# Kernel tuning notes

Measured on AMD Instinct MI355X. Metric: run time of the kernel, lower is better.

Reference implementation:

```python
import jax, jax.numpy as jnp
import numpy as np

B = 8192      # graphs per batch
NPG = 40      # nodes per graph (= average_nodes, uniform here)
DEG = 16      # avg degree
IN = 64
HID = 32
OUT = 10
K1 = 20       # ceil(0.5*40)
K2 = 10       # ceil(0.5*20)
N = B * NPG
E = N * DEG
EPS = 1e-15


def _lin_params(k, fi, fo):
    kw, kb = jax.random.split(k)
    s = 1.0 / np.sqrt(fi)
    w = jax.random.uniform(kw, (fi, fo), jnp.float32, -s, s)
    b = jax.random.uniform(kb, (fo,), jnp.float32, -s, s)
    return w, b


def setup_inputs():
    key = jax.random.key(0)
    ks = jax.random.split(key, 14)
    x = jax.random.normal(ks[0], (N, IN), jnp.float32)
    # edges constrained within each graph (graphs are contiguous blocks of NPG nodes)
    g = jnp.repeat(jnp.arange(B, dtype=jnp.int32), NPG * DEG)
    src = g * NPG + jax.random.randint(ks[1], (E,), 0, NPG, dtype=jnp.int32)
    dst = g * NPG + jax.random.randint(ks[2], (E,), 0, NPG, dtype=jnp.int32)
    edge_index = jnp.stack([src, dst])
    batch = jnp.repeat(jnp.arange(B, dtype=jnp.int32), NPG)
    w_c1, b_c1 = _lin_params(ks[3], IN, HID)
    w_p1, b_p1 = _lin_params(ks[4], HID, K1)
    w2r, b2 = _lin_params(ks[5], HID, HID)
    w2o, _ = _lin_params(ks[6], HID, HID)
    w_p2, b_p2 = _lin_params(ks[7], HID, K2)
    w3r, b3 = _lin_params(ks[8], HID, HID)
    w3o, _ = _lin_params(ks[9], HID, HID)
    w_l1, b_l1 = _lin_params(ks[10], HID, HID)
    w_l2, b_l2 = _lin_params(ks[11], HID, OUT)
    return dict(x=x, edge_index=edge_index, batch=batch,
                w_c1=w_c1, b_c1=b_c1, w_p1=w_p1, b_p1=b_p1,
                w2r=w2r, b2=b2, w2o=w2o, w_p2=w_p2, b_p2=b_p2,
                w3r=w3r, b3=b3, w3o=w3o,
                w_l1=w_l1, b_l1=b_l1, w_l2=w_l2, b_l2=b_l2)


def _gcn_conv(x, edge_index, w, b):
    # PyG GCNConv: x' = D^-1/2 (A + I) D^-1/2 (X W) + b, unit edge weights
    h = x @ w
    row, col = edge_index
    deg = jnp.zeros((N,), h.dtype).at[col].add(1.0) + 1.0  # +1 self loop
    dinv = jax.lax.rsqrt(deg)
    msg = (dinv[row] * dinv[col])[:, None] * h[row]
    out = jnp.zeros_like(h).at[col].add(msg)
    out = out + (dinv * dinv)[:, None] * h  # self-loop contribution
    return out + b


def _dense_mincut_pool(x, adj, s, mask=None):
    # faithful to torch_geometric.nn.dense_mincut_pool
    s = jax.nn.softmax(s, axis=-1)
    if mask is not None:
        m = mask[..., None].astype(x.dtype)
        x = x * m
        s = s * m
    k = s.shape[-1]
    out = jnp.einsum('bnk,bnf->bkf', s, x)
    out_adj = jnp.einsum('bnk,bnm,bml->bkl', s, adj, s)
    mincut_num = jnp.trace(out_adj, axis1=1, axis2=2)
    d_flat = adj.sum(-1)                                   # [B, n]
    mincut_den = jnp.einsum('bnk,bn,bnk->b', s, d_flat, s)  # tr(S^T D S)
    mincut_loss = jnp.mean(-(mincut_num / mincut_den))
    ss = jnp.einsum('bnk,bnl->bkl', s, s)
    ss_norm = jnp.sqrt(jnp.sum(ss * ss, axis=(1, 2), keepdims=True))
    i_s = jnp.eye(k, dtype=x.dtype) / jnp.sqrt(jnp.asarray(k, x.dtype))
    ortho_loss = jnp.mean(jnp.sqrt(jnp.sum((ss / ss_norm - i_s) ** 2, axis=(1, 2))))
    # zero diagonal, then symmetric degree-normalize coarse adjacency
    eye = jnp.eye(k, dtype=x.dtype)
    out_adj = out_adj * (1.0 - eye)
    d = jnp.sqrt(out_adj.sum(-1))[:, None, :] + EPS        # [B,1,k]
    out_adj = out_adj / d / jnp.swapaxes(d, 1, 2)
    return out, out_adj, mincut_loss, ortho_loss


def _dense_graph_conv(x, adj, w_rel, b, w_root):
    # PyG DenseGraphConv (aggr='add'): lin_rel(A @ x) + lin_root(x); lin_root bias=False
    return (adj @ x) @ w_rel + b + x @ w_root


def reference(x, edge_index, batch, w_c1, b_c1, w_p1, b_p1, w2r, b2, w2o,
              w_p2, b_p2, w3r, b3, w3o, w_l1, b_l1, w_l2, b_l2):
    h = jax.nn.relu(_gcn_conv(x, edge_index, w_c1, b_c1))
    # to_dense_batch (uniform NPG nodes per graph, batch sorted)
    local = jnp.arange(N, dtype=jnp.int32) - batch * NPG
    xd = jnp.zeros((B, NPG, HID), h.dtype).at[batch, local].set(h)
    mask = jnp.ones((B, NPG), bool)
    # to_dense_adj (accumulates duplicate edges)
    row, col = edge_index
    g = batch[row]
    adj = jnp.zeros((B, NPG, NPG), h.dtype).at[g, row - g * NPG, col - g * NPG].add(1.0)
    s = xd @ w_p1 + b_p1
    xd, adj, mc1, o1 = _dense_mincut_pool(xd, adj, s, mask)
    xd = jax.nn.relu(_dense_graph_conv(xd, adj, w2r, b2, w2o))
    s = xd @ w_p2 + b_p2
    xd, adj, mc2, o2 = _dense_mincut_pool(xd, adj, s)
    xd = _dense_graph_conv(xd, adj, w3r, b3, w3o)
    pooled = xd.mean(axis=1)
    out = jax.nn.relu(pooled @ w_l1 + b_l1) @ w_l2 + b_l2
    return out, mc1 + mc2 + o1 + o2
```

## Files before the change

kernel.cpp:

```cpp
#include <hip/hip_runtime.h>

#define NT 256

constexpr int Bg   = 8192;
constexpr int NPG  = 40;
constexpr int EPG  = 640;
constexpr int IN_  = 64;
constexpr int HID  = 32;
constexpr int K1   = 20;
constexpr int K2   = 10;
constexpr int OUTC = 10;
constexpr int NE   = Bg * NPG * 16;
constexpr int SH   = 36;
constexpr float EPSF = 1e-15f;

#define FMA4(acc, a, b) do { \
    float _s = (a); \
    acc.x = fmaf(_s, (b).x, acc.x); \
    acc.y = fmaf(_s, (b).y, acc.y); \
    acc.z = fmaf(_s, (b).z, acc.z); \
    acc.w = fmaf(_s, (b).w, acc.w); } while (0)

__device__ __forceinline__ float wave_red(float v) {
#pragma unroll
    for (int off = 32; off > 0; off >>= 1) v += __shfl_down(v, off, 64);
    return v;
}

__global__ __launch_bounds__(NT, 4)
void mincut_fused(const float* __restrict__ x, const int* __restrict__ ei,
                  const float* __restrict__ w_c1, const float* __restrict__ b_c1,
                  const float* __restrict__ w_p1, const float* __restrict__ b_p1,
                  const float* __restrict__ w2r_, const float* __restrict__ b2_,
                  const float* __restrict__ w2o_,
                  const float* __restrict__ w_p2, const float* __restrict__ b_p2,
                  const float* __restrict__ w3r_, const float* __restrict__ b3_,
                  const float* __restrict__ w3o_,
                  const float* __restrict__ w_l1, const float* __restrict__ b_l1,
                  const float* __restrict__ w_l2, const float* __restrict__ b_l2,
                  float* __restrict__ out, float* __restrict__ wsg)
{
    __shared__ __align__(16) float sA_[NPG * NPG];
    __shared__ __align__(16) float bufH[NPG * SH];
    __shared__ __align__(16) float bufXd[NPG * SH];
    __shared__ __align__(16) float bufS[NPG * K1];
    __shared__ __align__(16) float bufAS[NPG * K1];
    __shared__ __align__(16) float sSS[K1 * K1];
    __shared__ __align__(16) float sdinv[NPG];
    __shared__ __align__(16) float srowsA[NPG];
    __shared__ __align__(16) float srowm[NPG];
    __shared__ __align__(16) float sden[NPG];
    __shared__ __align__(16) float sred1[2];
    __shared__ __align__(16) float sred2[2];
    __shared__ __align__(16) float sc[8];

    float* sA2  = sA_;
    float* sX2  = bufH;
    float* sW2r = bufH + 720;
    float* sW2o = bufAS;
    float* sS2  = bufS;
    float* sAS2 = bufS + 200;
    float* sA3  = bufS + 400;
    float* sSS2 = bufS + 500;
    float* sW3r = bufXd;
    float* sW3o = bufXd + 360;
    float* sX3  = bufXd + 720;
    float* sX4  = bufXd + 1080;

    const int g    = blockIdx.x;
    const int tid  = threadIdx.x;
    const int lane = tid & 63;
    const int wid  = tid >> 6;

    int er0, ec0, er1, ec1, er2 = -1, ec2 = 0;
    {
        const int eb = g * EPG, nb = g * NPG;
        const int* srcp = ei;
        const int* dstp = ei + NE;
        int e = eb + tid;
        er0 = srcp[e] - nb; ec0 = dstp[e] - nb;
        e += NT;
        er1 = srcp[e] - nb; ec1 = dstp[e] - nb;
        if (tid + 2 * NT < EPG) {
            e += NT;
            er2 = srcp[e] - nb; ec2 = dstp[e] - nb;
        }
    }
    for (int i = tid; i < NPG * NPG; i += NT) sA_[i] = 0.f;
    __syncthreads();

    atomicAdd(&sA_[er0 * NPG + ec0], 1.f);
    atomicAdd(&sA_[er1 * NPG + ec1], 1.f);
    if (er2 >= 0) atomicAdd(&sA_[er2 * NPG + ec2], 1.f);

    if (tid < 160) {
        int np = tid >> 3, fq = tid & 7;
        int n0 = 2 * np, n1 = n0 + 1;
        const float4* x0 = (const float4*)(x + (size_t)g * (NPG * IN_) + n0 * IN_);
        const float4* x1 = (const float4*)(x + (size_t)g * (NPG * IN_) + n1 * IN_);
        const float4* wg = (const float4*)w_c1;
        float4 acc0 = {0.f,0.f,0.f,0.f}, acc1 = {0.f,0.f,0.f,0.f};
#pragma unroll 4
        for (int kk = 0; kk < IN_ / 4; kk++) {
            float4 a0 = x0[kk], a1 = x1[kk];
            float4 w0 = wg[(4*kk+0)*8 + fq];
            float4 w1 = wg[(4*kk+1)*8 + fq];
            float4 w2 = wg[(4*kk+2)*8 + fq];
            float4 w3 = wg[(4*kk+3)*8 + fq];
            FMA4(acc0, a0.x, w0); FMA4(acc0, a0.y, w1);
            FMA4(acc0, a0.z, w2); FMA4(acc0, a0.w, w3);
            FMA4(acc1, a1.x, w0); FMA4(acc1, a1.y, w1);
            FMA4(acc1, a1.z, w2); FMA4(acc1, a1.w, w3);
        }
        ((float4*)(bufH + n0 * SH))[fq] = acc0;
        ((float4*)(bufH + n1 * SH))[fq] = acc1;
    }
    __syncthreads();

    if (tid < NPG) {
        float s = 0.f;
#pragma unroll
        for (int r = 0; r < NPG; r++) s += sA_[r * NPG + tid];
        sdinv[tid] = rsqrtf(s + 1.f);
    } else if (tid >= 64 && tid < 64 + NPG) {
        int n = tid - 64; float s = 0.f;
#pragma unroll
        for (int m = 0; m < NPG; m++) s += sA_[n * NPG + m];
        srowsA[n] = s;
    }
    __syncthreads();

    if (tid < 160) {
        int cp = tid >> 3, fq = tid & 7;
        int c0 = 2 * cp, c1 = c0 + 1;
        float4 acc0 = {0.f,0.f,0.f,0.f}, acc1 = {0.f,0.f,0.f,0.f};
#pragma unroll 8
        for (int r = 0; r < NPG; r++) {
            float2 a2 = *(const float2*)&sA_[r * NPG + c0];
            float dv = sdinv[r];
            float4 b = ((const float4*)(bufH + r * SH))[fq];
            FMA4(acc0, a2.x * dv, b);
            FMA4(acc1, a2.y * dv, b);
        }
        float4 bb = ((const float4*)b_c1)[fq];
        float4 h0 = ((const float4*)(bufH + c0 * SH))[fq];
        float4 h1 = ((const float4*)(bufH + c1 * SH))[fq];
        float d0 = sdinv[c0], d1 = sdinv[c1];
        float4 r0, r1;
        r0.x = fmaxf(fmaf(d0, fmaf(d0, h0.x, acc0.x), bb.x), 0.f);
        r0.y = fmaxf(fmaf(d0, fmaf(d0, h0.y, acc0.y), bb.y), 0.f);
        r0.z = fmaxf(fmaf(d0, fmaf(d0, h0.z, acc0.z), bb.z), 0.f);
        r0.w = fmaxf(fmaf(d0, fmaf(d0, h0.w, acc0.w), bb.w), 0.f);
        r1.x = fmaxf(fmaf(d1, fmaf(d1, h1.x, acc1.x), bb.x), 0.f);
        r1.y = fmaxf(fmaf(d1, fmaf(d1, h1.y, acc1.y), bb.y), 0.f);
        r1.z = fmaxf(fmaf(d1, fmaf(d1, h1.z, acc1.z), bb.z), 0.f);
        r1.w = fmaxf(fmaf(d1, fmaf(d1, h1.w, acc1.w), bb.w), 0.f);
        ((float4*)(bufXd + c0 * SH))[fq] = r0;
        ((float4*)(bufXd + c1 * SH))[fq] = r1;
    }
    __syncthreads();

    if (tid < 100) {
        int np = tid / 5, lq = tid - np * 5;
        int n0 = 2 * np, n1 = n0 + 1;
        const float4* wg = (const float4*)w_p1;
        float4 bb = ((const float4*)b_p1)[lq];
        float4 acc0 = bb, acc1 = bb;
#pragma unroll 8
        for (int k = 0; k < HID; k++) {
            float a0 = bufXd[n0 * SH + k];
            float a1 = bufXd[n1 * SH + k];
            float4 w = wg[k * 5 + lq];
            FMA4(acc0, a0, w);
            FMA4(acc1, a1, w);
        }
        ((float4*)(bufS + n0 * K1))[lq] = acc0;
        ((float4*)(bufS + n1 * K1))[lq] = acc1;
    }
    __syncthreads();

    if (tid < NPG) {
        float* row = bufS + tid * K1;
        float v[K1]; float m = -3.0e38f;
#pragma unroll
        for (int k = 0; k < K1; k++) { v[k] = row[k]; m = fmaxf(m, v[k]); }
        float ssum = 0.f;
#pragma unroll
        for (int k = 0; k < K1; k++) { v[k] = __expf(v[k] - m); ssum += v[k]; }
        float inv = 1.f / ssum;
#pragma unroll
        for (int k = 0; k < K1; k++) row[k] = v[k] * inv;
    }
    __syncthreads();

    if (tid < 100) {
        int np = tid / 5, lq = tid - np * 5;
        int n0 = 2 * np, n1 = n0 + 1;
        const float4* sb = (const float4*)bufS;
        float4 acc0 = {0.f,0.f,0.f,0.f}, acc1 = {0.f,0.f,0.f,0.f};
#pragma unroll
        for (int m4 = 0; m4 < NPG / 4; m4++) {
            float4 a0 = *(const float4*)&sA_[n0 * NPG + 4 * m4];
            float4 a1 = *(const float4*)&sA_[n1 * NPG + 4 * m4];
            float4 b0 = sb[(4*m4+0)*5 + lq];
            float4 b1 = sb[(4*m4+1)*5 + lq];
            float4 b2v = sb[(4*m4+2)*5 + lq];
            float4 b3v = sb[(4*m4+3)*5 + lq];
            FMA4(acc0, a0.x, b0); FMA4(acc0, a0.y, b1);
            FMA4(acc0, a0.z, b2v); FMA4(acc0, a0.w, b3v);
            FMA4(acc1, a1.x, b0); FMA4(acc1, a1.y, b1);
            FMA4(acc1, a1.z, b2v); FMA4(acc1, a1.w, b3v);
        }
        ((float4*)(bufAS + n0 * K1))[lq] = acc0;
        ((float4*)(bufAS + n1 * K1))[lq] = acc1;
    } else if (tid < 150) {
        int oo = tid - 100;
        int kp = oo / 5, lq = oo - kp * 5;
        int k0 = 2 * kp, k1 = k0 + 1;
        float4 acc0 = {0.f,0.f,0.f,0.f}, acc1 = {0.f,0.f,0.f,0.f};
#pragma unroll 8
        for (int n = 0; n < NPG; n++) {
            float2 s2v = *(const float2*)&bufS[n * K1 + k0];
            float4 b = ((const float4*)(bufS + n * K1))[lq];
            FMA4(acc0, s2v.x, b);
            FMA4(acc1, s2v.y, b);
        }
        ((float4*)(sSS + k0 * K1))[lq] = acc0;
        ((float4*)(sSS + k1 * K1))[lq] = acc1;
    }
    __syncthreads();

    if (tid < 50) {
        int kp = tid / 5, lq = tid - kp * 5;
        int k0 = 2 * kp, k1 = k0 + 1;
        float4 acc0 = {0.f,0.f,0.f,0.f}, acc1 = {0.f,0.f,0.f,0.f};
#pragma unroll 8
        for (int n = 0; n < NPG; n++) {
            float2 s2v = *(const float2*)&bufS[n * K1 + k0];
            float4 b = ((const float4*)(bufAS + n * K1))[lq];
            FMA4(acc0, s2v.x, b);
            FMA4(acc1, s2v.y, b);
        }
        ((float4*)(sA2 + k0 * K1))[lq] = acc0;
        ((float4*)(sA2 + k1 * K1))[lq] = acc1;
    } else if (tid < 130) {
        int oo = tid - 50;
        int kp = oo >> 3, fq = oo & 7;
        int k0 = 2 * kp, k1 = k0 + 1;
        float4 acc0 = {0.f,0.f,0.f,0.f}, acc1 = {0.f,0.f,0.f,0.f};
#pragma unroll 8
        for (int n = 0; n < NPG; n++) {
            float2 s2v = *(const float2*)&bufS[n * K1 + k0];
            float4 b = ((const float4*)(bufXd + n * SH))[fq];
            FMA4(acc0, s2v.x, b);
            FMA4(acc1, s2v.y, b);
        }
        ((float4*)(sX2 + k0 * SH))[fq] = acc0;
        ((float4*)(sX2 + k1 * SH))[fq] = acc1;
    } else if (tid < 170) {
        int n = tid - 130;
        float s2 = 0.f;
#pragma unroll
        for (int k = 0; k < K1; k++) { float v = bufS[n * K1 + k]; s2 = fmaf(v, v, s2); }
        sden[n] = srowsA[n] * s2;
    } else if (wid == 3) {
        float v = 0.f;
        for (int i = lane; i < K1 * K1; i += 64) { float t = sSS[i]; v = fmaf(t, t, v); }
        v = wave_red(v); if (lane == 0) sc[2] = v;
    }
    __syncthreads();

    if (wid < 2) {
        float rn = 1.f / sqrtf(sc[2]);
        const float isk = 0.22360679774997896f;
        float p = 0.f;
        for (int o = tid; o < K1 * K1; o += 128) {
            int k = o / K1, l = o - k * K1;
            float v = sSS[o] * rn - ((k == l) ? isk : 0.f);
            p = fmaf(v, v, p);
        }
        p = wave_red(p);
        if (lane == 0) sred1[wid] = p;
    } else if (wid == 2) {
        float v = (lane < K1) ? sA2[lane * (K1 + 1)] : 0.f;
        v = wave_red(v); if (lane == 0) sc[0] = v;
        if (lane < K1) {
            float s = 0.f;
#pragma unroll
            for (int l = 0; l < K1; l++) s += sA2[lane * K1 + l];
            s -= sA2[lane * (K1 + 1)];
            srowm[lane] = 1.f / (sqrtf(s) + EPSF);
        }
    } else {
        float v = (lane < NPG) ? sden[lane] : 0.f;
        v = wave_red(v); if (lane == 0) sc[1] = v;
    }
    for (int o = tid; o < 320; o += NT) {
        bool first = (o < 160);
        int oo = first ? o : o - 160;
        int n = oo >> 3, fq = oo & 7;
        const float4* wg = (const float4*)(first ? w2r_ : w2o_);
        float4 acc = {0.f,0.f,0.f,0.f};
#pragma unroll 8
        for (int k = 0; k < HID; k++) {
            float a = sX2[n * SH + k];
            FMA4(acc, a, wg[k * 8 + fq]);
        }
        if (first) ((float4*)(sW2r + n * SH))[fq] = acc;
        else       ((float4*)(sW2o + n * SH))[fq] = acc;
    }
    __syncthreads();

    if (tid < 80) {
        int kp = tid >> 3, fq = tid & 7;
        int k0 = 2 * kp, k1 = k0 + 1;
        float4 acc0 = {0.f,0.f,0.f,0.f}, acc1 = {0.f,0.f,0.f,0.f};
#pragma unroll
        for (int l = 0; l < K1; l++) {
            float rl = srowm[l];
            float a0 = (l == k0) ? 0.f : sA2[k0 * K1 + l];
            float a1 = (l == k1) ? 0.f : sA2[k1 * K1 + l];
            float4 w = ((const float4*)(sW2r + l * SH))[fq];
            FMA4(acc0, a0 * rl, w);
            FMA4(acc1, a1 * rl, w);
        }
        float4 bb = ((const float4*)b2_)[fq];
        float4 o0 = ((const float4*)(sW2o + k0 * SH))[fq];
        float4 o1 = ((const float4*)(sW2o + k1 * SH))[fq];
        float rk0 = srowm[k0], rk1 = srowm[k1];
        float4 r0, r1;
        r0.x = fmaxf(fmaf(rk0, acc0.x, o0.x + bb.x), 0.f);
        r0.y = fmaxf(fmaf(rk0, acc0.y, o0.y + bb.y), 0.f);
        r0.z = fmaxf(fmaf(rk0, acc0.z, o0.z + bb.z), 0.f);
        r0.w = fmaxf(fmaf(rk0, acc0.w, o0.w + bb.w), 0.f);
        r1.x = fmaxf(fmaf(rk1, acc1.x, o1.x + bb.x), 0.f);
        r1.y = fmaxf(fmaf(rk1, acc1.y, o1.y + bb.y), 0.f);
        r1.z = fmaxf(fmaf(rk1, acc1.z, o1.z + bb.z), 0.f);
        r1.w = fmaxf(fmaf(rk1, acc1.w, o1.w + bb.w), 0.f);
        ((float4*)(sX2 + k0 * SH))[fq] = r0;
        ((float4*)(sX2 + k1 * SH))[fq] = r1;
    }
    __syncthreads();

    if (tid < K1 * K2) {
        int n = tid / K2, q = tid - n * K2;
        float acc = b_p2[q];
#pragma unroll 8
        for (int j = 0; j < HID; j++) acc = fmaf(sX2[n * SH + j], w_p2[j * K2 + q], acc);
        sS2[tid] = acc;
    }
    __syncthreads();

    if (tid < K1) {
        float* row = sS2 + tid * K2;
        float v[K2]; float m = -3.0e38f;
#pragma unroll
        for (int q = 0; q < K2; q++) { v[q] = row[q]; m = fmaxf(m, v[q]); }
        float ssum = 0.f;
#pragma unroll
        for (int q = 0; q < K2; q++) { v[q] = __expf(v[q] - m); ssum += v[q]; }
        float inv = 1.f / ssum;
#pragma unroll
        for (int q = 0; q < K2; q++) row[q] = v[q] * inv;
    }
    __syncthreads();

    for (int o = tid; o < 400; o += NT) {
        if (o < 200) {
            int n = o / K2, l = o - n * K2;
            float acc = 0.f;
#pragma unroll
            for (int m = 0; m < K1; m++) {
                float a = (m == n) ? 0.f : sA2[n * K1 + m];
                acc = fmaf(a * srowm[m], sS2[m * K2 + l], acc);
            }
            sAS2[n * K2 + l] = acc * srowm[n];
        } else if (o < 300) {
            int oo = o - 200; int k = oo / K2, l = oo - k * K2;
            float acc = 0.f;
#pragma unroll
            for (int n = 0; n < K1; n++) acc = fmaf(sS2[n * K2 + k], sS2[n * K2 + l], acc);
            sSS2[k * K2 + l] = acc;
        } else if (o < 380) {
            int oo = o - 300; int k = oo >> 3, fq = oo & 7;
            float4 acc = {0.f, 0.f, 0.f, 0.f};
#pragma unroll
            for (int n = 0; n < K1; n++) {
                float a = sS2[n * K2 + k];
                float4 b = ((const float4*)(sX2 + n * SH))[fq];
                FMA4(acc, a, b);
            }
            ((float4*)(sX3 + k * SH))[fq] = acc;
        } else {
            int n = o - 380;
            float da = 0.f, s2 = 0.f;
#pragma unroll
            for (int l = 0; l < K1; l++) {
                float a = (l == n) ? 0.f : sA2[n * K1 + l];
                da = fmaf(a, srowm[l], da);
            }
            da *= srowm[n];
#pragma unroll
            for (int q = 0; q < K2; q++) { float v = sS2[n * K2 + q]; s2 = fmaf(v, v, s2); }
            sden[n] = da * s2;
        }
    }
    __syncthreads();

    if (tid < K2 * K2) {
        int k = tid / K2, l = tid - k * K2;
        float acc = 0.f;
#pragma unroll
        for (int n = 0; n < K1; n++) acc = fmaf(sS2[n * K2 + k], sAS2[n * K2 + l], acc);
        sA3[tid] = acc;
    } else if (wid == 2) {
        float v = (lane < K1) ? sden[lane] : 0.f;
        v = wave_red(v); if (lane == 0) sc[5] = v;
    } else if (wid == 3) {
        float v = 0.f;
        for (int i = lane; i < K2 * K2; i += 64) { float t = sSS2[i]; v = fmaf(t, t, v); }
        v = wave_red(v); if (lane == 0) sc[6] = v;
    }
    __syncthreads();

    if (wid == 0) {
        float rn = 1.f / sqrtf(sc[6]);
        const float isk = 0.31622776601683794f;
        float p = 0.f;
        for (int i = lane; i < K2 * K2; i += 64) {
            int k = i / K2, l = i - k * K2;
            float v = sSS2[i] * rn - ((k == l) ? isk : 0.f);
            p = fmaf(v, v, p);
        }
        p = wave_red(p);
        if (lane == 0) sred2[0] = p;
    } else if (wid == 1) {
        float v = (lane < K2) ? sA3[lane * (K2 + 1)] : 0.f;
        v = wave_red(v); if (lane == 0) sc[4] = v;
        if (lane < K2) {
            float s = 0.f;
#pragma unroll
            for (int l = 0; l < K2; l++) s += sA3[lane * K2 + l];
            s -= sA3[lane * (K2 + 1)];
            srowm[lane] = 1.f / (sqrtf(s) + EPSF);
        }
    }
    __syncthreads();

    if (tid < 160) {
        bool first = (tid < 80);
        int oo = first ? tid : tid - 80;
        int n = oo >> 3, fq = oo & 7;
        const float4* wg = (const float4*)(first ? w3r_ : w3o_);
        float4 acc = {0.f,0.f,0.f,0.f};
#pragma unroll 8
        for (int k = 0; k < HID; k++) {
            float a = sX3[n * SH + k];
            FMA4(acc, a, wg[k * 8 + fq]);
        }
        if (first) ((float4*)(sW3r + n * SH))[fq] = acc;
        else       ((float4*)(sW3o + n * SH))[fq] = acc;
    } else if (tid == 200) {
        float o1 = sqrtf(sred1[0] + sred1[1]);
        float o2 = sqrtf(sred2[0]);
        wsg[g] = -(sc[0] / sc[1]) + o1 - (sc[4] / sc[5]) + o2;
    }
    __syncthreads();

    if (tid < 40) {
        int kp = tid >> 3, fq = tid & 7;
        int k0 = 2 * kp, k1 = k0 + 1;
        float4 acc0 = {0.f,0.f,0.f,0.f}, acc1 = {0.f,0.f,0.f,0.f};
#pragma unroll
        for (int l = 0; l < K2; l++) {
            float rl = srowm[l];
            float a0 = (l == k0) ? 0.f : sA3[k0 * K2 + l];
            float a1 = (l == k1) ? 0.f : sA3[k1 * K2 + l];
            float4 w = ((const float4*)(sW3r + l * SH))[fq];
            FMA4(acc0, a0 * rl, w);
            FMA4(acc1, a1 * rl, w);
        }
        float4 bb = ((const float4*)b3_)[fq];
        float4 o0 = ((const float4*)(sW3o + k0 * SH))[fq];
        float4 o1 = ((const float4*)(sW3o + k1 * SH))[fq];
        float rk0 = srowm[k0], rk1 = srowm[k1];
        float4 r0, r1;
        r0.x = fmaf(rk0, acc0.x, o0.x + bb.x);
        r0.y = fmaf(rk0, acc0.y, o0.y + bb.y);
        r0.z = fmaf(rk0, acc0.z, o0.z + bb.z);
        r0.w = fmaf(rk0, acc0.w, o0.w + bb.w);
        r1.x = fmaf(rk1, acc1.x, o1.x + bb.x);
        r1.y = fmaf(rk1, acc1.y, o1.y + bb.y);
        r1.z = fmaf(rk1, acc1.z, o1.z + bb.z);
        r1.w = fmaf(rk1, acc1.w, o1.w + bb.w);
        ((float4*)(sX4 + k0 * SH))[fq] = r0;
        ((float4*)(sX4 + k1 * SH))[fq] = r1;
    }
    __syncthreads();

    if (wid == 0) {
        int f = lane & 31;
        float pool = 0.f;
#pragma unroll
        for (int n = 0; n < K2; n++) pool += sX4[n * SH + f];
        pool *= (1.f / K2);
        float acc = b_l1[f];
#pragma unroll
        for (int j = 0; j < HID; j++)
            acc = fmaf(__shfl(pool, j, 64), w_l1[j * HID + f], acc);
        float t1 = fmaxf(acc, 0.f);
        int o = (lane < OUTC) ? lane : 0;
        float acc2 = b_l2[o];
#pragma unroll
        for (int j = 0; j < HID; j++)
            acc2 = fmaf(__shfl(t1, j, 64), w_l2[j * OUTC + o], acc2);
        if (lane < OUTC) out[(size_t)g * OUTC + lane] = acc2;
    }
}

__global__ void loss_reduce(const float* __restrict__ wsg, float* __restrict__ out)
{
    __shared__ float sred[4];
    int tid = threadIdx.x;
    float s = 0.f;
    for (int i = tid; i < Bg; i += NT) s += wsg[i];
    s = wave_red(s);
    if ((tid & 63) == 0) sred[tid >> 6] = s;
    __syncthreads();
    if (tid == 0) out[(size_t)Bg * OUTC] = (sred[0] + sred[1] + sred[2] + sred[3]) * (1.f / Bg);
}

extern "C" void kernel_launch(void* const* d_in, const int* in_sizes, int n_in,
                              void* d_out, int out_size, void* d_ws, size_t ws_size,
                              hipStream_t stream)
{
    const float* x    = (const float*)d_in[0];
    const int*   ei   = (const int*)  d_in[1];
    const float* w_c1 = (const float*)d_in[3];
    const float* b_c1 = (const float*)d_in[4];
    const float* w_p1 = (const float*)d_in[5];
    const float* b_p1 = (const float*)d_in[6];
    const float* w2r  = (const float*)d_in[7];
    const float* b2   = (const float*)d_in[8];
    const float* w2o  = (const float*)d_in[9];
    const float* w_p2 = (const float*)d_in[10];
    const float* b_p2 = (const float*)d_in[11];
    const float* w3r  = (const float*)d_in[12];
    const float* b3   = (const float*)d_in[13];
    const float* w3o  = (const float*)d_in[14];
    const float* w_l1 = (const float*)d_in[15];
    const float* b_l1 = (const float*)d_in[16];
    const float* w_l2 = (const float*)d_in[17];
    const float* b_l2 = (const float*)d_in[18];
    float* out = (float*)d_out;
    float* wsg = (float*)d_ws;

    hipLaunchKernelGGL(mincut_fused, dim3(Bg), dim3(NT), 0, stream,
                       x, ei, w_c1, b_c1, w_p1, b_p1, w2r, b2, w2o,
                       w_p2, b_p2, w3r, b3, w3o, w_l1, b_l1, w_l2, b_l2,
                       out, wsg);
    hipLaunchKernelGGL(loss_reduce, dim3(1), dim3(NT), 0, stream, wsg, out);
}
```

Before: 286.1 us.

## Process two graphs per block with a unified shared-memory arena

Each 256-thread block now handles two graphs instead of one, looping work items over both graphs so that idle threads in small phases are put to use. Shared memory becomes one flat arena with fixed offsets per graph, and the x tile is staged into LDS with coalesced float4 loads before the first linear layer. Several reductions are restructured into half-wave reductions and per-thread partial sums. The arena roughly doubles LDS per block (about 53 KB), which may cut occupancy, and the kernel launches half as many blocks.

New measurement: 314.9 us. +10.1%, slower.

```diff
diff --git a/kernel.cpp b/kernel.cpp
--- a/kernel.cpp
+++ b/kernel.cpp
@@ -14,12 +14,43 @@
 constexpr int SH   = 36;
 constexpr float EPSF = 1e-15f;
 
+constexpr int R = 6672;
+constexpr int AOFF   = 0;
+constexpr int HOFF   = 1600;
+constexpr int X2OFF  = 1600;
+constexpr int W2ROFF = 2320;
+constexpr int XdOFF  = 3040;
+constexpr int XOFF   = 3040;
+constexpr int W3ROFF = 3040;
+constexpr int W3OOFF = 3400;
+constexpr int X3OFF  = 3760;
+constexpr int X4OFF  = 4120;
+constexpr int SOFF   = 4480;
+constexpr int S2OFF  = 4480;
+constexpr int AS2OFF = 4680;
+constexpr int A3OFF  = 4880;
+constexpr int SS2OFF = 4980;
+constexpr int ASOFF  = 5280;
+constexpr int W2OOFF = 5280;
+constexpr int SSOFF  = 6080;
+constexpr int DINV   = 6480;
+constexpr int ROWSA  = 6520;
+constexpr int ROWM   = 6560;
+constexpr int SDEN   = 6600;
+constexpr int SC     = 6640;
+
 #define FMA4(acc, a, b) do { \
     float _s = (a); \
     acc.x = fmaf(_s, (b).x, acc.x); \
     acc.y = fmaf(_s, (b).y, acc.y); \
     acc.z = fmaf(_s, (b).z, acc.z); \
     acc.w = fmaf(_s, (b).w, acc.w); } while (0)
+
+__device__ __forceinline__ float hred32(float v) {
+#pragma unroll
+    for (int off = 16; off > 0; off >>= 1) v += __shfl_down(v, off, 32);
+    return v;
+}
 
 __device__ __forceinline__ float wave_red(float v) {
 #pragma unroll
@@ -40,64 +71,43 @@
                   const float* __restrict__ w_l2, const float* __restrict__ b_l2,
                   float* __restrict__ out, float* __restrict__ wsg)
 {
-    __shared__ __align__(16) float sA_[NPG * NPG];
-    __shared__ __align__(16) float bufH[NPG * SH];
-    __shared__ __align__(16) float bufXd[NPG * SH];
-    __shared__ __align__(16) float bufS[NPG * K1];
-    __shared__ __align__(16) float bufAS[NPG * K1];
-    __shared__ __align__(16) float sSS[K1 * K1];
-    __shared__ __align__(16) float sdinv[NPG];
-    __shared__ __align__(16) float srowsA[NPG];
-    __shared__ __align__(16) float srowm[NPG];
-    __shared__ __align__(16) float sden[NPG];
-    __shared__ __align__(16) float sred1[2];
-    __shared__ __align__(16) float sred2[2];
-    __shared__ __align__(16) float sc[8];
-
-    float* sA2  = sA_;
-    float* sX2  = bufH;
-    float* sW2r = bufH + 720;
-    float* sW2o = bufAS;
-    float* sS2  = bufS;
-    float* sAS2 = bufS + 200;
-    float* sA3  = bufS + 400;
-    float* sSS2 = bufS + 500;
-    float* sW3r = bufXd;
-    float* sW3o = bufXd + 360;
-    float* sX3  = bufXd + 720;
-    float* sX4  = bufXd + 1080;
-
-    const int g    = blockIdx.x;
+    __shared__ __align__(16) float sm[2 * R];
+
+    const int b    = blockIdx.x;
     const int tid  = threadIdx.x;
     const int lane = tid & 63;
     const int wid  = tid >> 6;
-
-    int er0, ec0, er1, ec1, er2 = -1, ec2 = 0;
+    const int hl   = tid & 31;
+    const int hw   = tid >> 5;
+
+    int aoff[5];
     {
-        const int eb = g * EPG, nb = g * NPG;
-        const int* srcp = ei;
-        const int* dstp = ei + NE;
-        int e = eb + tid;
-        er0 = srcp[e] - nb; ec0 = dstp[e] - nb;
-        e += NT;
-        er1 = srcp[e] - nb; ec1 = dstp[e] - nb;
-        if (tid + 2 * NT < EPG) {
-            e += NT;
-            er2 = srcp[e] - nb; ec2 = dstp[e] - nb;
-        }
-    }
-    for (int i = tid; i < NPG * NPG; i += NT) sA_[i] = 0.f;
-    __syncthreads();
-
-    atomicAdd(&sA_[er0 * NPG + ec0], 1.f);
-    atomicAdd(&sA_[er1 * NPG + ec1], 1.f);
-    if (er2 >= 0) atomicAdd(&sA_[er2 * NPG + ec2], 1.f);
-
-    if (tid < 160) {
-        int np = tid >> 3, fq = tid & 7;
-        int n0 = 2 * np, n1 = n0 + 1;
-        const float4* x0 = (const float4*)(x + (size_t)g * (NPG * IN_) + n0 * IN_);
-        const float4* x1 = (const float4*)(x + (size_t)g * (NPG * IN_) + n1 * IN_);
+        const int gi = tid >> 7;
+        const int nb = (2 * b + gi) * NPG;
+        const int base = gi * R;
+        const int e0 = b * 1280 + tid * 5;
+#pragma unroll
+        for (int j = 0; j < 5; j++) {
+            int r = ei[e0 + j] - nb, c = ei[NE + e0 + j] - nb;
+            aoff[j] = base + r * NPG + c;
+        }
+    }
+    for (int o = tid; o < 3200; o += NT) sm[(o < 1600) ? o : (R + o - 1600)] = 0.f;
+    for (int o = tid; o < 1280; o += NT) {
+        int gi = o >= 640; int i = o - 640 * gi;
+        int n = i >> 4, k = i & 15;
+        ((float4*)(sm + gi * R + XOFF + n * 68))[k] =
+            ((const float4*)(x + (size_t)(2 * b + gi) * (NPG * IN_)))[i];
+    }
+    __syncthreads();
+
+#pragma unroll
+    for (int j = 0; j < 5; j++) atomicAdd(&sm[aoff[j]], 1.f);
+    for (int o = tid; o < 320; o += NT) {
+        int gi = o >= 160; int oo = o - 160 * gi; float* G = sm + gi * R;
+        int np = oo >> 3, fq = oo & 7, n0 = 2 * np, n1 = n0 + 1;
+        const float4* x0 = (const float4*)(G + XOFF + n0 * 68);
+        const float4* x1 = (const float4*)(G + XOFF + n1 * 68);
         const float4* wg = (const float4*)w_c1;
         float4 acc0 = {0.f,0.f,0.f,0.f}, acc1 = {0.f,0.f,0.f,0.f};
 #pragma unroll 4
@@ -112,40 +122,43 @@
             FMA4(acc1, a1.x, w0); FMA4(acc1, a1.y, w1);
             FMA4(acc1, a1.z, w2); FMA4(acc1, a1.w, w3);
         }
-        ((float4*)(bufH + n0 * SH))[fq] = acc0;
-        ((float4*)(bufH + n1 * SH))[fq] = acc1;
-    }
-    __syncthreads();
-
-    if (tid < NPG) {
-        float s = 0.f;
-#pragma unroll
-        for (int r = 0; r < NPG; r++) s += sA_[r * NPG + tid];
-        sdinv[tid] = rsqrtf(s + 1.f);
-    } else if (tid >= 64 && tid < 64 + NPG) {
-        int n = tid - 64; float s = 0.f;
-#pragma unroll
-        for (int m = 0; m < NPG; m++) s += sA_[n * NPG + m];
-        srowsA[n] = s;
-    }
-    __syncthreads();
-
-    if (tid < 160) {
-        int cp = tid >> 3, fq = tid & 7;
-        int c0 = 2 * cp, c1 = c0 + 1;
+        ((float4*)(G + HOFF + n0 * SH))[fq] = acc0;
+        ((float4*)(G + HOFF + n1 * SH))[fq] = acc1;
+    }
+    __syncthreads();
+
+    for (int o = tid; o < 160; o += NT) {
+        int gi = o >= 80; int oo = o - 80 * gi; float* G = sm + gi * R;
+        if (oo < NPG) {
+            float s = 0.f;
+#pragma unroll
+            for (int r = 0; r < NPG; r++) s += G[r * NPG + oo];
+            G[DINV + oo] = rsqrtf(s + 1.f);
+        } else {
+            int n = oo - NPG; float s = 0.f;
+#pragma unroll
+            for (int m = 0; m < NPG; m++) s += G[n * NPG + m];
+            G[ROWSA + n] = s;
+        }
+    }
+    __syncthreads();
+
+    for (int o = tid; o < 320; o += NT) {
+        int gi = o >= 160; int oo = o - 160 * gi; float* G = sm + gi * R;
+        int cp = oo >> 3, fq = oo & 7, c0 = 2 * cp, c1 = c0 + 1;
         float4 acc0 = {0.f,0.f,0.f,0.f}, acc1 = {0.f,0.f,0.f,0.f};
 #pragma unroll 8
         for (int r = 0; r < NPG; r++) {
-            float2 a2 = *(const float2*)&sA_[r * NPG + c0];
-            float dv = sdinv[r];
-            float4 b = ((const float4*)(bufH + r * SH))[fq];
-            FMA4(acc0, a2.x * dv, b);
-            FMA4(acc1, a2.y * dv, b);
+            float2 a2 = *(const float2*)&G[r * NPG + c0];
+            float dv = G[DINV + r];
+            float4 bv = ((const float4*)(G + HOFF + r * SH))[fq];
+            FMA4(acc0, a2.x * dv, bv);
+            FMA4(acc1, a2.y * dv, bv);
         }
         float4 bb = ((const float4*)b_c1)[fq];
-        float4 h0 = ((const float4*)(bufH + c0 * SH))[fq];
-        float4 h1 = ((const float4*)(bufH + c1 * SH))[fq];
-        float d0 = sdinv[c0], d1 = sdinv[c1];
+        float4 h0 = ((const float4*)(G + HOFF + c0 * SH))[fq];
+        float4 h1 = ((const float4*)(G + HOFF + c1 * SH))[fq];
+        float d0 = G[DINV + c0], d1 = G[DINV + c1];
         float4 r0, r1;
         r0.x = fmaxf(fmaf(d0, fmaf(d0, h0.x, acc0.x), bb.x), 0.f);
         r0.y = fmaxf(fmaf(d0, fmaf(d0, h0.y, acc0.y), bb.y), 0.f);
@@ -155,32 +168,32 @@
         r1.y = fmaxf(fmaf(d1, fmaf(d1, h1.y, acc1.y), bb.y), 0.f);
         r1.z = fmaxf(fmaf(d1, fmaf(d1, h1.z, acc1.z), bb.z), 0.f);
         r1.w = fmaxf(fmaf(d1, fmaf(d1, h1.w, acc1.w), bb.w), 0.f);
-        ((float4*)(bufXd + c0 * SH))[fq] = r0;
-        ((float4*)(bufXd + c1 * SH))[fq] = r1;
-    }
-    __syncthreads();
-
-    if (tid < 100) {
-        int np = tid / 5, lq = tid - np * 5;
-        int n0 = 2 * np, n1 = n0 + 1;
+        ((float4*)(G + XdOFF + c0 * SH))[fq] = r0;
+        ((float4*)(G + XdOFF + c1 * SH))[fq] = r1;
+    }
+    __syncthreads();
+
+    for (int o = tid; o < 200; o += NT) {
+        int gi = o >= 100; int oo = o - 100 * gi; float* G = sm + gi * R;
+        int np = oo / 5, lq = oo - np * 5, n0 = 2 * np, n1 = n0 + 1;
         const float4* wg = (const float4*)w_p1;
         float4 bb = ((const float4*)b_p1)[lq];
         float4 acc0 = bb, acc1 = bb;
 #pragma unroll 8
         for (int k = 0; k < HID; k++) {
-            float a0 = bufXd[n0 * SH + k];
-            float a1 = bufXd[n1 * SH + k];
+            float a0 = G[XdOFF + n0 * SH + k];
+            float a1 = G[XdOFF + n1 * SH + k];
             float4 w = wg[k * 5 + lq];
-            FMA4(acc0, a0, w);
-            FMA4(acc1, a1, w);
-        }
-        ((float4*)(bufS + n0 * K1))[lq] = acc0;
-        ((float4*)(bufS + n1 * K1))[lq] = acc1;
-    }
-    __syncthreads();
-
-    if (tid < NPG) {
-        float* row = bufS + tid * K1;
+            FMA4(acc0, a0, w); FMA4(acc1, a1, w);
+        }
+        ((float4*)(G + SOFF + n0 * K1))[lq] = acc0;
+        ((float4*)(G + SOFF + n1 * K1))[lq] = acc1;
+    }
+    __syncthreads();
+
+    if (tid < 80) {
+        int gi = tid >= 40; int n = tid - 40 * gi;
+        float* row = sm + gi * R + SOFF + n * K1;
         float v[K1]; float m = -3.0e38f;
 #pragma unroll
         for (int k = 0; k < K1; k++) { v[k] = row[k]; m = fmaxf(m, v[k]); }
@@ -193,141 +206,139 @@
     }
     __syncthreads();
 
-    if (tid < 100) {
-        int np = tid / 5, lq = tid - np * 5;
-        int n0 = 2 * np, n1 = n0 + 1;
-        const float4* sb = (const float4*)bufS;
-        float4 acc0 = {0.f,0.f,0.f,0.f}, acc1 = {0.f,0.f,0.f,0.f};
-#pragma unroll
-        for (int m4 = 0; m4 < NPG / 4; m4++) {
-            float4 a0 = *(const float4*)&sA_[n0 * NPG + 4 * m4];
-            float4 a1 = *(const float4*)&sA_[n1 * NPG + 4 * m4];
-            float4 b0 = sb[(4*m4+0)*5 + lq];
-            float4 b1 = sb[(4*m4+1)*5 + lq];
-            float4 b2v = sb[(4*m4+2)*5 + lq];
-            float4 b3v = sb[(4*m4+3)*5 + lq];
-            FMA4(acc0, a0.x, b0); FMA4(acc0, a0.y, b1);
-            FMA4(acc0, a0.z, b2v); FMA4(acc0, a0.w, b3v);
-            FMA4(acc1, a1.x, b0); FMA4(acc1, a1.y, b1);
-            FMA4(acc1, a1.z, b2v); FMA4(acc1, a1.w, b3v);
-        }
-        ((float4*)(bufAS + n0 * K1))[lq] = acc0;
-        ((float4*)(bufAS + n1 * K1))[lq] = acc1;
-    } else if (tid < 150) {
-        int oo = tid - 100;
-        int kp = oo / 5, lq = oo - kp * 5;
-        int k0 = 2 * kp, k1 = k0 + 1;
-        float4 acc0 = {0.f,0.f,0.f,0.f}, acc1 = {0.f,0.f,0.f,0.f};
-#pragma unroll 8
-        for (int n = 0; n < NPG; n++) {
-            float2 s2v = *(const float2*)&bufS[n * K1 + k0];
-            float4 b = ((const float4*)(bufS + n * K1))[lq];
-            FMA4(acc0, s2v.x, b);
-            FMA4(acc1, s2v.y, b);
-        }
-        ((float4*)(sSS + k0 * K1))[lq] = acc0;
-        ((float4*)(sSS + k1 * K1))[lq] = acc1;
-    }
-    __syncthreads();
-
-    if (tid < 50) {
-        int kp = tid / 5, lq = tid - kp * 5;
-        int k0 = 2 * kp, k1 = k0 + 1;
-        float4 acc0 = {0.f,0.f,0.f,0.f}, acc1 = {0.f,0.f,0.f,0.f};
-#pragma unroll 8
-        for (int n = 0; n < NPG; n++) {
-            float2 s2v = *(const float2*)&bufS[n * K1 + k0];
-            float4 b = ((const float4*)(bufAS + n * K1))[lq];
-            FMA4(acc0, s2v.x, b);
-            FMA4(acc1, s2v.y, b);
-        }
-        ((float4*)(sA2 + k0 * K1))[lq] = acc0;
-        ((float4*)(sA2 + k1 * K1))[lq] = acc1;
-    } else if (tid < 130) {
-        int oo = tid - 50;
-        int kp = oo >> 3, fq = oo & 7;
-        int k0 = 2 * kp, k1 = k0 + 1;
-        float4 acc0 = {0.f,0.f,0.f,0.f}, acc1 = {0.f,0.f,0.f,0.f};
-#pragma unroll 8
-        for (int n = 0; n < NPG; n++) {
-            float2 s2v = *(const float2*)&bufS[n * K1 + k0];
-            float4 b = ((const float4*)(bufXd + n * SH))[fq];
-            FMA4(acc0, s2v.x, b);
-            FMA4(acc1, s2v.y, b);
-        }
-        ((float4*)(sX2 + k0 * SH))[fq] = acc0;
-        ((float4*)(sX2 + k1 * SH))[fq] = acc1;
-    } else if (tid < 170) {
-        int n = tid - 130;
-        float s2 = 0.f;
-#pragma unroll
-        for (int k = 0; k < K1; k++) { float v = bufS[n * K1 + k]; s2 = fmaf(v, v, s2); }
-        sden[n] = srowsA[n] * s2;
-    } else if (wid == 3) {
+    for (int o = tid; o < 300; o += NT) {
+        int gi = o >= 150; int oo = o - 150 * gi; float* G = sm + gi * R;
+        if (oo < 100) {
+            int np = oo / 5, lq = oo - np * 5, n0 = 2 * np, n1 = n0 + 1;
+            const float4* sb = (const float4*)(G + SOFF);
+            float4 acc0 = {0.f,0.f,0.f,0.f}, acc1 = {0.f,0.f,0.f,0.f};
+#pragma unroll
+            for (int m4 = 0; m4 < NPG / 4; m4++) {
+                float4 a0 = *(const float4*)&G[n0 * NPG + 4 * m4];
+                float4 a1 = *(const float4*)&G[n1 * NPG + 4 * m4];
+                float4 b0 = sb[(4*m4+0)*5 + lq];
+                float4 b1 = sb[(4*m4+1)*5 + lq];
+                float4 b2v = sb[(4*m4+2)*5 + lq];
+                float4 b3v = sb[(4*m4+3)*5 + lq];
+                FMA4(acc0, a0.x, b0); FMA4(acc0, a0.y, b1);
+                FMA4(acc0, a0.z, b2v); FMA4(acc0, a0.w, b3v);
+                FMA4(acc1, a1.x, b0); FMA4(acc1, a1.y, b1);
+                FMA4(acc1, a1.z, b2v); FMA4(acc1, a1.w, b3v);
+            }
+            ((float4*)(G + ASOFF + n0 * K1))[lq] = acc0;
+            ((float4*)(G + ASOFF + n1 * K1))[lq] = acc1;
+        } else {
+            int m = oo - 100;
+            int kp = m / 5, lq = m - kp * 5, k0 = 2 * kp, k1 = k0 + 1;
+            float4 acc0 = {0.f,0.f,0.f,0.f}, acc1 = {0.f,0.f,0.f,0.f};
+#pragma unroll 8
+            for (int n = 0; n < NPG; n++) {
+                float2 s2v = *(const float2*)&G[SOFF + n * K1 + k0];
+                float4 bv = ((const float4*)(G + SOFF + n * K1))[lq];
+                FMA4(acc0, s2v.x, bv); FMA4(acc1, s2v.y, bv);
+            }
+            ((float4*)(G + SSOFF + k0 * K1))[lq] = acc0;
+            ((float4*)(G + SSOFF + k1 * K1))[lq] = acc1;
+        }
+    }
+    __syncthreads();
+
+    for (int o = tid; o < 340; o += NT) {
+        int gi = o >= 170; int oo = o - 170 * gi; float* G = sm + gi * R;
+        if (oo < 50) {
+            int kp = oo / 5, lq = oo - kp * 5, k0 = 2 * kp, k1 = k0 + 1;
+            float4 acc0 = {0.f,0.f,0.f,0.f}, acc1 = {0.f,0.f,0.f,0.f};
+#pragma unroll 8
+            for (int n = 0; n < NPG; n++) {
+                float2 s2v = *(const float2*)&G[SOFF + n * K1 + k0];
+                float4 bv = ((const float4*)(G + ASOFF + n * K1))[lq];
+                FMA4(acc0, s2v.x, bv); FMA4(acc1, s2v.y, bv);
+            }
+            ((float4*)(G + AOFF + k0 * K1))[lq] = acc0;
+            ((float4*)(G + AOFF + k1 * K1))[lq] = acc1;
+        } else if (oo < 130) {
+            int m = oo - 50;
+            int kp = m >> 3, fq = m & 7, k0 = 2 * kp, k1 = k0 + 1;
+            float4 acc0 = {0.f,0.f,0.f,0.f}, acc1 = {0.f,0.f,0.f,0.f};
+#pragma unroll 8
+            for (int n = 0; n < NPG; n++) {
+                float2 s2v = *(const float2*)&G[SOFF + n * K1 + k0];
+                float4 bv = ((const float4*)(G + XdOFF + n * SH))[fq];
+                FMA4(acc0, s2v.x, bv); FMA4(acc1, s2v.y, bv);
+            }
+            ((float4*)(G + X2OFF + k0 * SH))[fq] = acc0;
+            ((float4*)(G + X2OFF + k1 * SH))[fq] = acc1;
+        } else {
+            int n = oo - 130;
+            float s2 = 0.f;
+#pragma unroll
+            for (int k = 0; k < K1; k++) { float v = G[SOFF + n * K1 + k]; s2 = fmaf(v, v, s2); }
+            G[SDEN + n] = G[ROWSA + n] * s2;
+        }
+    }
+    __syncthreads();
+
+    if (hw < 2) {
+        float* G = sm + hw * R;
+        float f = 0.f, tr = 0.f;
+        for (int i = hl; i < K1 * K1; i += 32) {
+            float t = G[SSOFF + i];
+            f = fmaf(t, t, f);
+            if (i % (K1 + 1) == 0) tr += t;
+        }
+        f = hred32(f); tr = hred32(tr);
+        if (hl == 0)
+            G[SC + 2] = sqrtf(fmaxf(2.f - 2.f * tr / (sqrtf(f) * 4.47213595499958f), 0.f));
+    } else if (hw < 4) {
+        float* G = sm + (hw - 2) * R;
         float v = 0.f;
-        for (int i = lane; i < K1 * K1; i += 64) { float t = sSS[i]; v = fmaf(t, t, v); }
-        v = wave_red(v); if (lane == 0) sc[2] = v;
-    }
-    __syncthreads();
-
-    if (wid < 2) {
-        float rn = 1.f / sqrtf(sc[2]);
-        const float isk = 0.22360679774997896f;
-        float p = 0.f;
-        for (int o = tid; o < K1 * K1; o += 128) {
-            int k = o / K1, l = o - k * K1;
-            float v = sSS[o] * rn - ((k == l) ? isk : 0.f);
-            p = fmaf(v, v, p);
-        }
-        p = wave_red(p);
-        if (lane == 0) sred1[wid] = p;
-    } else if (wid == 2) {
-        float v = (lane < K1) ? sA2[lane * (K1 + 1)] : 0.f;
-        v = wave_red(v); if (lane == 0) sc[0] = v;
-        if (lane < K1) {
+        if (hl < K1) {
             float s = 0.f;
 #pragma unroll
-            for (int l = 0; l < K1; l++) s += sA2[lane * K1 + l];
-            s -= sA2[lane * (K1 + 1)];
-            srowm[lane] = 1.f / (sqrtf(s) + EPSF);
-        }
-    } else {
-        float v = (lane < NPG) ? sden[lane] : 0.f;
-        v = wave_red(v); if (lane == 0) sc[1] = v;
-    }
-    for (int o = tid; o < 320; o += NT) {
-        bool first = (o < 160);
-        int oo = first ? o : o - 160;
-        int n = oo >> 3, fq = oo & 7;
+            for (int l = 0; l < K1; l++) s += G[AOFF + hl * K1 + l];
+            float d = G[AOFF + hl * (K1 + 1)];
+            G[ROWM + hl] = 1.f / (sqrtf(s - d) + EPSF);
+            v = d;
+        }
+        v = hred32(v);
+        if (hl == 0) G[SC + 0] = v;
+    } else if (hw < 6) {
+        float* G = sm + (hw - 4) * R;
+        float v = G[SDEN + hl] + ((hl < 8) ? G[SDEN + hl + 32] : 0.f);
+        v = hred32(v);
+        if (hl == 0) G[SC + 1] = v;
+    }
+    for (int o = tid; o < 640; o += NT) {
+        int gi = o >= 320; int oo = o - 320 * gi; float* G = sm + gi * R;
+        int first = oo < 160; int m = first ? oo : oo - 160;
+        int n = m >> 3, fq = m & 7;
         const float4* wg = (const float4*)(first ? w2r_ : w2o_);
         float4 acc = {0.f,0.f,0.f,0.f};
 #pragma unroll 8
         for (int k = 0; k < HID; k++) {
-            float a = sX2[n * SH + k];
+            float a = G[X2OFF + n * SH + k];
             FMA4(acc, a, wg[k * 8 + fq]);
         }
-        if (first) ((float4*)(sW2r + n * SH))[fq] = acc;
-        else       ((float4*)(sW2o + n * SH))[fq] = acc;
-    }
-    __syncthreads();
-
-    if (tid < 80) {
-        int kp = tid >> 3, fq = tid & 7;
-        int k0 = 2 * kp, k1 = k0 + 1;
+        ((float4*)(G + (first ? W2ROFF : W2OOFF) + n * SH))[fq] = acc;
+    }
+    __syncthreads();
+
+    for (int o = tid; o < 160; o += NT) {
+        int gi = o >= 80; int oo = o - 80 * gi; float* G = sm + gi * R;
+        int kp = oo >> 3, fq = oo & 7, k0 = 2 * kp, k1 = k0 + 1;
         float4 acc0 = {0.f,0.f,0.f,0.f}, acc1 = {0.f,0.f,0.f,0.f};
 #pragma unroll
         for (int l = 0; l < K1; l++) {
-            float rl = srowm[l];
-            float a0 = (l == k0) ? 0.f : sA2[k0 * K1 + l];
-            float a1 = (l == k1) ? 0.f : sA2[k1 * K1 + l];
-            float4 w = ((const float4*)(sW2r + l * SH))[fq];
-            FMA4(acc0, a0 * rl, w);
-            FMA4(acc1, a1 * rl, w);
+            float rl = G[ROWM + l];
+            float a0 = (l == k0) ? 0.f : G[AOFF + k0 * K1 + l];
+            float a1 = (l == k1) ? 0.f : G[AOFF + k1 * K1 + l];
+            float4 w = ((const float4*)(G + W2ROFF + l * SH))[fq];
+            FMA4(acc0, a0 * rl, w); FMA4(acc1, a1 * rl, w);
         }
         float4 bb = ((const float4*)b2_)[fq];
-        float4 o0 = ((const float4*)(sW2o + k0 * SH))[fq];
-        float4 o1 = ((const float4*)(sW2o + k1 * SH))[fq];
-        float rk0 = srowm[k0], rk1 = srowm[k1];
+        float4 o0 = ((const float4*)(G + W2OOFF + k0 * SH))[fq];
+        float4 o1 = ((const float4*)(G + W2OOFF + k1 * SH))[fq];
+        float rk0 = G[ROWM + k0], rk1 = G[ROWM + k1];
         float4 r0, r1;
         r0.x = fmaxf(fmaf(rk0, acc0.x, o0.x + bb.x), 0.f);
         r0.y = fmaxf(fmaf(rk0, acc0.y, o0.y + bb.y), 0.f);
@@ -337,22 +348,24 @@
         r1.y = fmaxf(fmaf(rk1, acc1.y, o1.y + bb.y), 0.f);
         r1.z = fmaxf(fmaf(rk1, acc1.z, o1.z + bb.z), 0.f);
         r1.w = fmaxf(fmaf(rk1, acc1.w, o1.w + bb.w), 0.f);
-        ((float4*)(sX2 + k0 * SH))[fq] = r0;
-        ((float4*)(sX2 + k1 * SH))[fq] = r1;
-    }
-    __syncthreads();
-
-    if (tid < K1 * K2) {
-        int n = tid / K2, q = tid - n * K2;
+        ((float4*)(G + X2OFF + k0 * SH))[fq] = r0;
+        ((float4*)(G + X2OFF + k1 * SH))[fq] = r1;
+    }
+    __syncthreads();
+
+    for (int o = tid; o < 400; o += NT) {
+        int gi = o >= 200; int oo = o - 200 * gi; float* G = sm + gi * R;
+        int n = oo / K2, q = oo - n * K2;
         float acc = b_p2[q];
 #pragma unroll 8
-        for (int j = 0; j < HID; j++) acc = fmaf(sX2[n * SH + j], w_p2[j * K2 + q], acc);
-        sS2[tid] = acc;
-    }
-    __syncthreads();
-
-    if (tid < K1) {
-        float* row = sS2 + tid * K2;
+        for (int j = 0; j < HID; j++) acc = fmaf(G[X2OFF + n * SH + j], w_p2[j * K2 + q], acc);
+        G[S2OFF + oo] = acc;
+    }
+    __syncthreads();
+
+    if (tid < 40) {
+        int gi = tid >= 20; int n = tid - 20 * gi;
+        float* row = sm + gi * R + S2OFF + n * K2;
         float v[K2]; float m = -3.0e38f;
 #pragma unroll
         for (int q = 0; q < K2; q++) { v[q] = row[q]; m = fmaxf(m, v[q]); }
@@ -365,125 +378,125 @@
     }
     __syncthreads();
 
-    for (int o = tid; o < 400; o += NT) {
-        if (o < 200) {
-            int n = o / K2, l = o - n * K2;
+    for (int o = tid; o < 840; o += NT) {
+        int gi = o >= 420; int oo = o - 420 * gi; float* G = sm + gi * R;
+        if (oo < 200) {
+            int n = oo / K2, l = oo - n * K2;
             float acc = 0.f;
 #pragma unroll
             for (int m = 0; m < K1; m++) {
-                float a = (m == n) ? 0.f : sA2[n * K1 + m];
-                acc = fmaf(a * srowm[m], sS2[m * K2 + l], acc);
-            }
-            sAS2[n * K2 + l] = acc * srowm[n];
-        } else if (o < 300) {
-            int oo = o - 200; int k = oo / K2, l = oo - k * K2;
+                float a = (m == n) ? 0.f : G[AOFF + n * K1 + m];
+                acc = fmaf(a * G[ROWM + m], G[S2OFF + m * K2 + l], acc);
+            }
+            G[AS2OFF + oo] = acc * G[ROWM + n];
+        } else if (oo < 300) {
+            int m = oo - 200; int k = m / K2, l = m - k * K2;
             float acc = 0.f;
 #pragma unroll
-            for (int n = 0; n < K1; n++) acc = fmaf(sS2[n * K2 + k], sS2[n * K2 + l], acc);
-            sSS2[k * K2 + l] = acc;
-        } else if (o < 380) {
-            int oo = o - 300; int k = oo >> 3, fq = oo & 7;
-            float4 acc = {0.f, 0.f, 0.f, 0.f};
+            for (int n = 0; n < K1; n++) acc = fmaf(G[S2OFF + n * K2 + k], G[S2OFF + n * K2 + l], acc);
+            G[SS2OFF + m] = acc;
+        } else if (oo < 380) {
+            int m = oo - 300; int k = m >> 3, fq = m & 7;
+            float4 acc = {0.f,0.f,0.f,0.f};
 #pragma unroll
             for (int n = 0; n < K1; n++) {
-                float a = sS2[n * K2 + k];
-                float4 b = ((const float4*)(sX2 + n * SH))[fq];
-                FMA4(acc, a, b);
-            }
-            ((float4*)(sX3 + k * SH))[fq] = acc;
+                float a = G[S2OFF + n * K2 + k];
+                float4 bv = ((const float4*)(G + X2OFF + n * SH))[fq];
+                FMA4(acc, a, bv);
+            }
+            ((float4*)(G + X3OFF + k * SH))[fq] = acc;
         } else {
-            int n = o - 380;
+            int n = oo - 380;
             float da = 0.f, s2 = 0.f;
 #pragma unroll
             for (int l = 0; l < K1; l++) {
-                float a = (l == n) ? 0.f : sA2[n * K1 + l];
-                da = fmaf(a, srowm[l], da);
-            }
-            da *= srowm[n];
-#pragma unroll
-            for (int q = 0; q < K2; q++) { float v = sS2[n * K2 + q]; s2 = fmaf(v, v, s2); }
-            sden[n] = da * s2;
-        }
-    }
-    __syncthreads();
-
-    if (tid < K2 * K2) {
-        int k = tid / K2, l = tid - k * K2;
+                float a = (l == n) ? 0.f : G[AOFF + n * K1 + l];
+                da = fmaf(a, G[ROWM + l], da);
+            }
+            da *= G[ROWM + n];
+#pragma unroll
+            for (int q = 0; q < K2; q++) { float v = G[S2OFF + n * K2 + q]; s2 = fmaf(v, v, s2); }
+            G[SDEN + n] = da * s2;
+        }
+    }
+    __syncthreads();
+
+    if (tid < 200) {
+        int gi = tid >= 100; int oo = tid - 100 * gi; float* G = sm + gi * R;
+        int k = oo / K2, l = oo - k * K2;
         float acc = 0.f;
 #pragma unroll
-        for (int n = 0; n < K1; n++) acc = fmaf(sS2[n * K2 + k], sAS2[n * K2 + l], acc);
-        sA3[tid] = acc;
-    } else if (wid == 2) {
-        float v = (lane < K1) ? sden[lane] : 0.f;
-        v = wave_red(v); if (lane == 0) sc[5] = v;
-    } else if (wid == 3) {
-        float v = 0.f;
-        for (int i = lane; i < K2 * K2; i += 64) { float t = sSS2[i]; v = fmaf(t, t, v); }
-        v = wave_red(v); if (lane == 0) sc[6] = v;
-    }
-    __syncthreads();
-
-    if (wid == 0) {
-        float rn = 1.f / sqrtf(sc[6]);
-        const float isk = 0.31622776601683794f;
-        float p = 0.f;
-        for (int i = lane; i < K2 * K2; i += 64) {
-            int k = i / K2, l = i - k * K2;
-            float v = sSS2[i] * rn - ((k == l) ? isk : 0.f);
-            p = fmaf(v, v, p);
-        }
-        p = wave_red(p);
-        if (lane == 0) sred2[0] = p;
-    } else if (wid == 1) {
-        float v = (lane < K2) ? sA3[lane * (K2 + 1)] : 0.f;
-        v = wave_red(v); if (lane == 0) sc[4] = v;
-        if (lane < K2) {
-            float s = 0.f;
-#pragma unroll
-            for (int l = 0; l < K2; l++) s += sA3[lane * K2 + l];
-            s -= sA3[lane * (K2 + 1)];
-            srowm[lane] = 1.f / (sqrtf(s) + EPSF);
-        }
-    }
-    __syncthreads();
-
-    if (tid < 160) {
-        bool first = (tid < 80);
-        int oo = first ? tid : tid - 80;
-        int n = oo >> 3, fq = oo & 7;
+        for (int n = 0; n < K1; n++) acc = fmaf(G[S2OFF + n * K2 + k], G[AS2OFF + n * K2 + l], acc);
+        G[A3OFF + oo] = acc;
+    } else if (tid == 200 || tid == 201) {
+        float* G = sm + (tid - 200) * R;
+        float s = 0.f;
+#pragma unroll
+        for (int l = 0; l < K1; l++) s += G[SDEN + l];
+        G[SC + 3] = s;
+    } else if (tid >= 204 && tid < 212) {
+        int j = tid - 204; float* G = sm + (j >> 2) * R; int t = j & 3;
+        float f = 0.f, tr = 0.f;
+        for (int i = 25 * t; i < 25 * t + 25; i++) {
+            float v = G[SS2OFF + i];
+            f = fmaf(v, v, f);
+            if (i % (K2 + 1) == 0) tr += v;
+        }
+        G[SC + 8 + t] = f; G[SC + 12 + t] = tr;
+    }
+    __syncthreads();
+
+    if (tid < 10 || (tid >= 32 && tid < 42)) {
+        int gi = tid >= 32; int l = tid - 32 * gi; float* G = sm + gi * R;
+        float s = 0.f;
+#pragma unroll
+        for (int m = 0; m < K2; m++) s += G[A3OFF + l * K2 + m];
+        s -= G[A3OFF + l * (K2 + 1)];
+        G[ROWM + l] = 1.f / (sqrtf(s) + EPSF);
+    } else if (tid == 64 || tid == 65) {
+        int gi = tid - 64; float* G = sm + gi * R;
+        float f  = G[SC+8] + G[SC+9] + G[SC+10] + G[SC+11];
+        float tr = G[SC+12] + G[SC+13] + G[SC+14] + G[SC+15];
+        float o2 = sqrtf(fmaxf(2.f - 2.f * tr / (sqrtf(f) * 3.1622776601683795f), 0.f));
+        float num2 = 0.f;
+#pragma unroll
+        for (int k = 0; k < K2; k++) num2 += G[A3OFF + k * (K2 + 1)];
+        float loss = -(G[SC+0] / G[SC+1]) + G[SC+2] - num2 / G[SC+3] + o2;
+        wsg[2 * b + gi] = loss;
+    }
+    __syncthreads();
+
+    for (int o = tid; o < 320; o += NT) {
+        int gi = o >= 160; int oo = o - 160 * gi; float* G = sm + gi * R;
+        int first = oo < 80; int m = first ? oo : oo - 80;
+        int n = m >> 3, fq = m & 7;
         const float4* wg = (const float4*)(first ? w3r_ : w3o_);
         float4 acc = {0.f,0.f,0.f,0.f};
 #pragma unroll 8
         for (int k = 0; k < HID; k++) {
-            float a = sX3[n * SH + k];
+            float a = G[X3OFF + n * SH + k];
             FMA4(acc, a, wg[k * 8 + fq]);
         }
-        if (first) ((float4*)(sW3r + n * SH))[fq] = acc;
-        else       ((float4*)(sW3o + n * SH))[fq] = acc;
-    } else if (tid == 200) {
-        float o1 = sqrtf(sred1[0] + sred1[1]);
-        float o2 = sqrtf(sred2[0]);
-        wsg[g] = -(sc[0] / sc[1]) + o1 - (sc[4] / sc[5]) + o2;
-    }
-    __syncthreads();
-
-    if (tid < 40) {
-        int kp = tid >> 3, fq = tid & 7;
-        int k0 = 2 * kp, k1 = k0 + 1;
+        ((float4*)(G + (first ? W3ROFF : W3OOFF) + n * SH))[fq] = acc;
+    }
+    __syncthreads();
+
+    if (tid < 80) {
+        int gi = tid >= 40; int oo = tid - 40 * gi; float* G = sm + gi * R;
+        int kp = oo >> 3, fq = oo & 7, k0 = 2 * kp, k1 = k0 + 1;
         float4 acc0 = {0.f,0.f,0.f,0.f}, acc1 = {0.f,0.f,0.f,0.f};
 #pragma unroll
         for (int l = 0; l < K2; l++) {
-            float rl = srowm[l];
-            float a0 = (l == k0) ? 0.f : sA3[k0 * K2 + l];
-            float a1 = (l == k1) ? 0.f : sA3[k1 * K2 + l];
-            float4 w = ((const float4*)(sW3r + l * SH))[fq];
-            FMA4(acc0, a0 * rl, w);
-            FMA4(acc1, a1 * rl, w);
+            float rl = G[ROWM + l];
+            float a0 = (l == k0) ? 0.f : G[A3OFF + k0 * K2 + l];
+            float a1 = (l == k1) ? 0.f : G[A3OFF + k1 * K2 + l];
+            float4 w = ((const float4*)(G + W3ROFF + l * SH))[fq];
+            FMA4(acc0, a0 * rl, w); FMA4(acc1, a1 * rl, w);
         }
         float4 bb = ((const float4*)b3_)[fq];
-        float4 o0 = ((const float4*)(sW3o + k0 * SH))[fq];
-        float4 o1 = ((const float4*)(sW3o + k1 * SH))[fq];
-        float rk0 = srowm[k0], rk1 = srowm[k1];
+        float4 o0 = ((const float4*)(G + W3OOFF + k0 * SH))[fq];
+        float4 o1 = ((const float4*)(G + W3OOFF + k1 * SH))[fq];
+        float rk0 = G[ROWM + k0], rk1 = G[ROWM + k1];
         float4 r0, r1;
         r0.x = fmaf(rk0, acc0.x, o0.x + bb.x);
         r0.y = fmaf(rk0, acc0.y, o0.y + bb.y);
@@ -493,16 +506,17 @@
         r1.y = fmaf(rk1, acc1.y, o1.y + bb.y);
         r1.z = fmaf(rk1, acc1.z, o1.z + bb.z);
         r1.w = fmaf(rk1, acc1.w, o1.w + bb.w);
-        ((float4*)(sX4 + k0 * SH))[fq] = r0;
-        ((float4*)(sX4 + k1 * SH))[fq] = r1;
-    }
-    __syncthreads();
-
-    if (wid == 0) {
+        ((float4*)(G + X4OFF + k0 * SH))[fq] = r0;
+        ((float4*)(G + X4OFF + k1 * SH))[fq] = r1;
+    }
+    __syncthreads();
+
+    if (wid < 2) {
+        int gi = wid; float* G = sm + gi * R;
         int f = lane & 31;
         float pool = 0.f;
 #pragma unroll
-        for (int n = 0; n < K2; n++) pool += sX4[n * SH + f];
+        for (int n = 0; n < K2; n++) pool += G[X4OFF + n * SH + f];
         pool *= (1.f / K2);
         float acc = b_l1[f];
 #pragma unroll
@@ -514,7 +528,7 @@
 #pragma unroll
         for (int j = 0; j < HID; j++)
             acc2 = fmaf(__shfl(t1, j, 64), w_l2[j * OUTC + o], acc2);
-        if (lane < OUTC) out[(size_t)g * OUTC + lane] = acc2;
+        if (lane < OUTC) out[(size_t)(2 * b + gi) * OUTC + lane] = acc2;
     }
 }
 
@@ -555,7 +569,7 @@
     float* out = (float*)d_out;
     float* wsg = (float*)d_ws;
 
-    hipLaunchKernelGGL(mincut_fused, dim3(Bg), dim3(NT), 0, stream,
+    hipLaunchKernelGGL(mincut_fused, dim3(Bg / 2), dim3(NT), 0, stream,
                        x, ei, w_c1, b_c1, w_p1, b_p1, w2r, b2, w2o,
                        w_p2, b_p2, w3r, b3, w3o, w_l1, b_l1, w_l2, b_l2,
                        out, wsg);
```
